# Kernel optimization log

Hardware: AMD Instinct MI355X
Metric: run time of the kernel (lower is better)

Reference implementation:

```python
import jax, jax.numpy as jnp
import numpy as np
from jax import lax

B, IMG, P, CIN = 8, 224, 16, 3
D, NH, E, HID, DEPTH, NC = 768, 12, 4, 3072, 12, 1000
NPAT = (IMG // P) ** 2  # 196
S = NPAT + 1            # 197 tokens incl cls
HD = D // NH            # 64
EPS = 1e-5


def _ln(x, g, b):
    m = jnp.mean(x, axis=-1, keepdims=True)
    v = jnp.mean((x - m) ** 2, axis=-1, keepdims=True)
    return (x - m) * lax.rsqrt(v + EPS) * g + b


def setup_inputs() -> dict:
    key = jax.random.key(0)
    ks = list(jax.random.split(key, 24))
    def rn(k, shape, s=0.02):
        return (jax.random.normal(k, shape) * s).astype(jnp.float32)
    inp = {
        "x": jax.random.normal(ks[0], (B, CIN, IMG, IMG), dtype=jnp.float32),
        "patch_w": rn(ks[1], (D, CIN, P, P)),
        "patch_b": jnp.zeros((D,), jnp.float32),
        "cls_token": jnp.zeros((1, 1, D), jnp.float32),
        "pos_embed": rn(ks[2], (1, S, D)),
        "ln1_g": jnp.ones((DEPTH, D), jnp.float32),
        "ln1_b": jnp.zeros((DEPTH, D), jnp.float32),
        "ln2_g": jnp.ones((DEPTH, D), jnp.float32),
        "ln2_b": jnp.zeros((DEPTH, D), jnp.float32),
        "attn_in_w": rn(ks[3], (DEPTH, 3 * D, D)),
        "attn_in_b": jnp.zeros((DEPTH, 3 * D), jnp.float32),
        "attn_out_w": rn(ks[4], (DEPTH, D, D)),
        "attn_out_b": jnp.zeros((DEPTH, D), jnp.float32),
        "gate_w": rn(ks[5], (DEPTH, E, D)),
        "gate_b": jnp.zeros((DEPTH, E), jnp.float32),
        "w1": rn(ks[6], (DEPTH, E, D, HID)),
        "b1": jnp.zeros((DEPTH, E, HID), jnp.float32),
        "w2": rn(ks[7], (DEPTH, E, HID, D)),
        "b2": jnp.zeros((DEPTH, E, D), jnp.float32),
        "head_w": rn(ks[8], (NC, D)),
        "head_b": jnp.zeros((NC,), jnp.float32),
    }
    return inp


def _forward(x, patch_w, patch_b, cls_token, pos_embed, ln1_g, ln1_b, ln2_g, ln2_b,
             attn_in_w, attn_in_b, attn_out_w, attn_out_b, gate_w, gate_b,
             w1, b1, w2, b2, head_w, head_b):
    # Patch embedding: conv stride=patch, then flatten spatial -> tokens
    feat = lax.conv_general_dilated(x, patch_w, window_strides=(P, P), padding="VALID",
                                    dimension_numbers=("NCHW", "OIHW", "NCHW"))
    t = feat.reshape(B, D, NPAT).transpose(0, 2, 1) + patch_b  # [B, 196, D]
    cls = jnp.broadcast_to(cls_token, (B, 1, D))
    h = jnp.concatenate([cls, t], axis=1) + pos_embed  # [B, S, D]

    scale = 1.0 / np.sqrt(HD).astype(np.float32)
    for i in range(DEPTH):
        # ---- attention (query = LN(x); key/value = x, as in source) ----
        qn = _ln(h, ln1_g[i], ln1_b[i])
        wq, wk, wv = attn_in_w[i, :D], attn_in_w[i, D:2 * D], attn_in_w[i, 2 * D:]
        bq, bk, bv = attn_in_b[i, :D], attn_in_b[i, D:2 * D], attn_in_b[i, 2 * D:]
        q = (qn @ wq.T + bq).reshape(B, S, NH, HD)
        k = (h @ wk.T + bk).reshape(B, S, NH, HD)
        v = (h @ wv.T + bv).reshape(B, S, NH, HD)
        scores = jnp.einsum("bqhd,bkhd->bhqk", q, k) * scale
        attn = jax.nn.softmax(scores, axis=-1)
        o = jnp.einsum("bhqk,bkhd->bqhd", attn, v).reshape(B, S, D)
        h = h + o @ attn_out_w[i].T + attn_out_b[i]

        # ---- Top-1 gated MoE MLP ----
        y = _ln(h, ln2_g[i], ln2_b[i])
        logits = y @ gate_w[i].T + gate_b[i]            # [B,S,E]
        probs = jax.nn.softmax(logits, axis=-1)
        top = jnp.argmax(probs, axis=-1)                # [B,S]
        onehot = jax.nn.one_hot(top, E, dtype=y.dtype)  # [B,S,E]
        gv = jnp.sum(probs * onehot, axis=-1)           # [B,S] top-1 gate score
        hidd = jax.nn.gelu(jnp.einsum("bsd,edh->besh", y, w1[i]) + b1[i][None, :, None, :])
        eout = jnp.einsum("besh,ehd->besd", hidd, w2[i]) + b2[i][None, :, None, :]
        moe = jnp.einsum("bse,besd->bsd", onehot, eout) * gv[..., None]
        h = h + moe

    return h[:, 0] @ head_w.T + head_b  # [B, NC]


def reference(x, patch_w, patch_b, cls_token, pos_embed, ln1_g, ln1_b, ln2_g, ln2_b,
              attn_in_w, attn_in_b, attn_out_w, attn_out_b, gate_w, gate_b,
              w1, b1, w2, b2, head_w, head_b):
    return _forward(x, patch_w, patch_b, cls_token, pos_embed, ln1_g, ln1_b, ln2_g,
                    ln2_b, attn_in_w, attn_in_b, attn_out_w, attn_out_b, gate_w,
                    gate_b, w1, b1, w2, b2, head_w, head_b)
```

## Files before the change

kernel.cpp:

```cpp
#include <hip/hip_runtime.h>
#include <math.h>


#define BB 8
#define SS 197
#define DD 768
#define MT (BB*SS)
#define NPATCH 196
#define MPE (BB*NPATCH)
#define HHID 3072
#define NEXP 4

typedef __bf16 bf16_t;
typedef bf16_t bf16x8 __attribute__((ext_vector_type(8)));
typedef float  f32x4  __attribute__((ext_vector_type(4)));

__device__ __forceinline__ void gload16(const bf16_t* g, bf16_t* l) {
    __builtin_amdgcn_global_load_lds(
        (const __attribute__((address_space(1))) unsigned int*)g,
        (__attribute__((address_space(3))) unsigned int*)l,
        16, 0, 0);
}

__device__ __forceinline__ bf16x8 cvt8(float4 a, float4 b) {
    bf16x8 o;
    o[0]=(bf16_t)a.x; o[1]=(bf16_t)a.y; o[2]=(bf16_t)a.z; o[3]=(bf16_t)a.w;
    o[4]=(bf16_t)b.x; o[5]=(bf16_t)b.y; o[6]=(bf16_t)b.z; o[7]=(bf16_t)b.w;
    return o;
}

__global__ void gather_patches(const float* __restrict__ x, bf16_t* __restrict__ Xp) {
    int i = blockIdx.x * 256 + threadIdx.x;
    if (i >= MPE * DD) return;
    int k = i % DD;
    int m = i / DD;
    int pw = k & 15, ph = (k >> 4) & 15, cin = k >> 8;
    int px = m % 14, py = (m / 14) % 14, b = m / NPATCH;
    int row = py * 16 + ph, col = px * 16 + pw;
    Xp[i] = (bf16_t)x[((size_t)(b * 3 + cin) * 224 + row) * 224 + col];
}

__global__ void build_h(const float* __restrict__ pe, const float* __restrict__ patch_b,
                        const float* __restrict__ cls, const float* __restrict__ pos,
                        float* __restrict__ h) {
    int i = blockIdx.x * 256 + threadIdx.x;
    if (i >= MT * DD) return;
    int d = i % DD;
    int s = (i / DD) % SS;
    int b = i / (DD * SS);
    float v;
    if (s == 0) v = cls[d];
    else        v = pe[((size_t)(b * NPATCH) + (s - 1)) * DD + d] + patch_b[d];
    h[i] = v + pos[s * DD + d];
}

__global__ void cvt_bf16(const float* __restrict__ in, bf16_t* __restrict__ out, int n) {
    int i = (blockIdx.x * 256 + threadIdx.x) * 8;
    if (i >= n) return;
    const float4* p = (const float4*)(in + i);
    *(bf16x8*)(out + i) = cvt8(p[0], p[1]);
}

__global__ __launch_bounds__(256) void transpose_cvt(const float* __restrict__ in,
                                                     bf16_t* __restrict__ out, int R, int C) {
    int z = blockIdx.z;
    in  += (size_t)z * R * C;
    out += (size_t)z * R * C;
    __shared__ float t[32][33];
    int c0 = blockIdx.x * 32, r0 = blockIdx.y * 32;
    int tx = threadIdx.x & 31, ty = threadIdx.x >> 5;
    #pragma unroll
    for (int i = 0; i < 4; i++)
        t[ty + 8*i][tx] = in[(size_t)(r0 + ty + 8*i) * C + c0 + tx];
    __syncthreads();
    #pragma unroll
    for (int i = 0; i < 4; i++)
        out[(size_t)(c0 + ty + 8*i) * R + r0 + tx] = (bf16_t)t[tx][ty + 8*i];
}

template<int MODE>
__global__ __launch_bounds__(256) void gemm_bf16(
    const bf16_t* __restrict__ A, const bf16_t* __restrict__ Bw,
    const float* __restrict__ bias, float* __restrict__ C, bf16_t* __restrict__ Cb,
    const int* __restrict__ cnt, const int* __restrict__ idx,
    const float* __restrict__ gv, int M, int N, int K)
{
    constexpr bool GATHER = (MODE == 3 || MODE == 4);
    int z = blockIdx.z;
    int count = GATHER ? cnt[z] : M;
    int m0 = blockIdx.y * 64;
    if (m0 >= count) return;
    int n0 = blockIdx.x * 64;
    Bw += (size_t)z * N * K;
    const float* biasz = bias ? (bias + (size_t)z * N) : nullptr;

    __shared__ bf16_t As[2][64 * 64];
    __shared__ bf16_t Bs[2][64 * 64];
    __shared__ int toks[64];

    int tid = threadIdx.x, lane = tid & 63, w = tid >> 6;
    if (tid < 64) {
        int mm = m0 + tid;
        if (mm > count - 1) mm = count - 1;
        toks[tid] = GATHER ? idx[z * MT + mm] : mm;
    }
    __syncthreads();

    int wm = (w >> 1) * 32, wn = (w & 1) * 32;
    int fr = lane & 15, fs = lane >> 4;

    f32x4 acc[2][2];
    #pragma unroll
    for (int mi = 0; mi < 2; mi++)
        #pragma unroll
        for (int ni = 0; ni < 2; ni++)
            #pragma unroll
            for (int j = 0; j < 4; j++) acc[mi][ni][j] = 0.f;

    int nk = K >> 6;

    #define STAGE(buf, k0)                                                          \
        {                                                                           \
            _Pragma("unroll")                                                       \
            for (int it = 0; it < 2; it++) {                                        \
                int row = 8*(it*4 + w) + (lane >> 3), cc = lane & 7;                \
                const bf16_t* sa = A  + (size_t)toks[row] * K + (k0) + ((cc ^ (row & 7)) << 3); \
                gload16(sa, &As[buf][(it*4 + w) * 512]);                            \
                const bf16_t* sb = Bw + (size_t)(n0 + row) * K + (k0) + ((cc ^ (row & 7)) << 3); \
                gload16(sb, &Bs[buf][(it*4 + w) * 512]);                            \
            }                                                                       \
        }

    STAGE(0, 0);
    __syncthreads();
    int cur = 0;
    for (int t = 0; t < nk; t++) {
        if (t + 1 < nk) STAGE(cur ^ 1, (t + 1) << 6);
        #pragma unroll
        for (int ks = 0; ks < 2; ks++) {
            bf16x8 af[2], bfr[2];
            #pragma unroll
            for (int mi = 0; mi < 2; mi++) {
                int r = wm + mi * 16 + fr;
                af[mi] = *(bf16x8*)&As[cur][r * 64 + (((fs + ks*4) ^ (r & 7)) << 3)];
            }
            #pragma unroll
            for (int ni = 0; ni < 2; ni++) {
                int r = wn + ni * 16 + fr;
                bfr[ni] = *(bf16x8*)&Bs[cur][r * 64 + (((fs + ks*4) ^ (r & 7)) << 3)];
            }
            #pragma unroll
            for (int mi = 0; mi < 2; mi++)
                #pragma unroll
                for (int ni = 0; ni < 2; ni++)
                    acc[mi][ni] = __builtin_amdgcn_mfma_f32_16x16x32_bf16(af[mi], bfr[ni], acc[mi][ni], 0, 0, 0);
        }
        __syncthreads();
        cur ^= 1;
    }
    #undef STAGE

    #pragma unroll
    for (int mi = 0; mi < 2; mi++) {
        #pragma unroll
        for (int j = 0; j < 4; j++) {
            int rr = wm + mi * 16 + fs * 4 + j;
            if (m0 + rr >= count) continue;
            int crow = toks[rr];
            #pragma unroll
            for (int ni = 0; ni < 2; ni++) {
                int col = n0 + wn + ni * 16 + fr;
                float v = acc[mi][ni][j];
                if (MODE >= 2) v += biasz[col];
                if (MODE == 0) C[(size_t)crow * N + col] = v;
                else if (MODE == 2) C[(size_t)crow * N + col] += v;
                else if (MODE == 3) {
                    float g = 0.5f * v * (1.0f + tanhf(0.7978845608028654f * (v + 0.044715f * v * v * v)));
                    Cb[(size_t)crow * N + col] = (bf16_t)g;
                } else if (MODE == 4) {
                    C[(size_t)crow * N + col] += v * gv[crow];
                } else {
                    Cb[(size_t)crow * N + col] = (bf16_t)v;
                }
            }
        }
    }
}

__global__ __launch_bounds__(256) void ln1_kernel(const float* __restrict__ x,
                                                  const float* __restrict__ g,
                                                  const float* __restrict__ b,
                                                  bf16_t* __restrict__ qn,
                                                  bf16_t* __restrict__ hb)
{
    int m = blockIdx.x, t = threadIdx.x;
    __shared__ float buf[DD];
    __shared__ float tmp[4];
    float s = 0.f;
    for (int j = t; j < DD; j += 256) { float v = x[(size_t)m*DD + j]; buf[j] = v; s += v; }
    #pragma unroll
    for (int o = 32; o > 0; o >>= 1) s += __shfl_down(s, o);
    if ((t & 63) == 0) tmp[t >> 6] = s;
    __syncthreads();
    float mean = (tmp[0]+tmp[1]+tmp[2]+tmp[3]) * (1.0f/DD);
    float s2 = 0.f;
    for (int j = t; j < DD; j += 256) { float d = buf[j] - mean; s2 += d*d; }
    #pragma unroll
    for (int o = 32; o > 0; o >>= 1) s2 += __shfl_down(s2, o);
    __syncthreads();
    if ((t & 63) == 0) tmp[t >> 6] = s2;
    __syncthreads();
    float var = (tmp[0]+tmp[1]+tmp[2]+tmp[3]) * (1.0f/DD);
    float rs = rsqrtf(var + 1e-5f);
    for (int j = t; j < DD; j += 256) {
        qn[(size_t)m*DD + j] = (bf16_t)((buf[j] - mean) * rs * g[j] + b[j]);
        hb[(size_t)m*DD + j] = (bf16_t)buf[j];
    }
}

__global__ __launch_bounds__(256) void ln2_gate_kernel(const float* __restrict__ x,
                                                       const float* __restrict__ g,
                                                       const float* __restrict__ b,
                                                       const float* __restrict__ gw,
                                                       const float* __restrict__ gb,
                                                       bf16_t* __restrict__ yb,
                                                       float* __restrict__ gv,
                                                       int* __restrict__ cnt,
                                                       int* __restrict__ idxb)
{
    int m = blockIdx.x, t = threadIdx.x;
    __shared__ float buf[DD];
    __shared__ float tmp[4];
    __shared__ float red[4][4];
    float s = 0.f;
    for (int j = t; j < DD; j += 256) { float v = x[(size_t)m*DD + j]; buf[j] = v; s += v; }
    #pragma unroll
    for (int o = 32; o > 0; o >>= 1) s += __shfl_down(s, o);
    if ((t & 63) == 0) tmp[t >> 6] = s;
    __syncthreads();
    float mean = (tmp[0]+tmp[1]+tmp[2]+tmp[3]) * (1.0f/DD);
    float s2 = 0.f;
    for (int j = t; j < DD; j += 256) { float d = buf[j] - mean; s2 += d*d; }
    #pragma unroll
    for (int o = 32; o > 0; o >>= 1) s2 += __shfl_down(s2, o);
    __syncthreads();
    if ((t & 63) == 0) tmp[t >> 6] = s2;
    __syncthreads();
    float var = (tmp[0]+tmp[1]+tmp[2]+tmp[3]) * (1.0f/DD);
    float rs = rsqrtf(var + 1e-5f);
    float p0 = 0.f, p1 = 0.f, p2 = 0.f, p3 = 0.f;
    for (int j = t; j < DD; j += 256) {
        float y = (buf[j] - mean) * rs * g[j] + b[j];
        yb[(size_t)m*DD + j] = (bf16_t)y;
        p0 += y * gw[j];
        p1 += y * gw[DD + j];
        p2 += y * gw[2*DD + j];
        p3 += y * gw[3*DD + j];
    }
    #pragma unroll
    for (int o = 32; o > 0; o >>= 1) {
        p0 += __shfl_down(p0, o); p1 += __shfl_down(p1, o);
        p2 += __shfl_down(p2, o); p3 += __shfl_down(p3, o);
    }
    if ((t & 63) == 0) { int ww = t >> 6; red[ww][0]=p0; red[ww][1]=p1; red[ww][2]=p2; red[ww][3]=p3; }
    __syncthreads();
    if (t == 0) {
        float l0 = red[0][0]+red[1][0]+red[2][0]+red[3][0] + gb[0];
        float l1 = red[0][1]+red[1][1]+red[2][1]+red[3][1] + gb[1];
        float l2 = red[0][2]+red[1][2]+red[2][2]+red[3][2] + gb[2];
        float l3 = red[0][3]+red[1][3]+red[2][3]+red[3][3] + gb[3];
        int top = 0; float best = l0;
        if (l1 > best) { best = l1; top = 1; }
        if (l2 > best) { best = l2; top = 2; }
        if (l3 > best) { best = l3; top = 3; }
        float Z = __expf(l0-best) + __expf(l1-best) + __expf(l2-best) + __expf(l3-best);
        gv[m] = 1.0f / Z;
        int pos = atomicAdd(&cnt[top], 1);
        idxb[top * MT + pos] = m;
    }
}

__global__ __launch_bounds__(256) void attn_kernel(const bf16_t* __restrict__ qb,
                                                   const bf16_t* __restrict__ kvb,
                                                   bf16_t* __restrict__ ob)
{
    int qt = blockIdx.x, hh = blockIdx.y, b = blockIdx.z;
    __shared__ bf16_t Qs[64 * 64];
    __shared__ bf16_t Ks[64 * 64];
    __shared__ bf16_t Vt[64 * 72];
    __shared__ float  Sc[64 * 276];
    __shared__ float  linv[64];

    int tid = threadIdx.x, lane = tid & 63, w = tid >> 6;
    int wm = (w >> 1) * 32, wn = (w & 1) * 32;
    int fr = lane & 15, fs = lane >> 4;

    #pragma unroll
    for (int it = 0; it < 2; it++) {
        int row = 8*(it*4 + w) + (lane >> 3), cc = lane & 7;
        int q = qt*64 + row; if (q > SS-1) q = SS-1;
        const bf16_t* src = qb + ((size_t)(b*SS + q))*DD + hh*64 + ((cc ^ (row & 7)) << 3);
        gload16(src, &Qs[(it*4 + w) * 512]);
    }

    for (int kt = 0; kt < 4; kt++) {
        __syncthreads();
        #pragma unroll
        for (int it = 0; it < 2; it++) {
            int row = 8*(it*4 + w) + (lane >> 3), cc = lane & 7;
            int k = kt*64 + row; if (k > SS-1) k = SS-1;
            const bf16_t* src = kvb + ((size_t)(b*SS + k))*1536 + hh*64 + ((cc ^ (row & 7)) << 3);
            gload16(src, &Ks[(it*4 + w) * 512]);
        }
        __syncthreads();
        f32x4 acc[2][2];
        #pragma unroll
        for (int mi = 0; mi < 2; mi++)
            #pragma unroll
            for (int ni = 0; ni < 2; ni++)
                #pragma unroll
                for (int j = 0; j < 4; j++) acc[mi][ni][j] = 0.f;
        #pragma unroll
        for (int ks = 0; ks < 2; ks++) {
            bf16x8 af[2], bfr[2];
            #pragma unroll
            for (int mi = 0; mi < 2; mi++) {
                int r = wm + mi * 16 + fr;
                af[mi] = *(bf16x8*)&Qs[r * 64 + (((fs + ks*4) ^ (r & 7)) << 3)];
            }
            #pragma unroll
            for (int ni = 0; ni < 2; ni++) {
                int r = wn + ni * 16 + fr;
                bfr[ni] = *(bf16x8*)&Ks[r * 64 + (((fs + ks*4) ^ (r & 7)) << 3)];
            }
            #pragma unroll
            for (int mi = 0; mi < 2; mi++)
                #pragma unroll
                for (int ni = 0; ni < 2; ni++)
                    acc[mi][ni] = __builtin_amdgcn_mfma_f32_16x16x32_bf16(af[mi], bfr[ni], acc[mi][ni], 0, 0, 0);
        }
        #pragma unroll
        for (int mi = 0; mi < 2; mi++)
            #pragma unroll
            for (int j = 0; j < 4; j++) {
                int qr = wm + mi * 16 + fs * 4 + j;
                #pragma unroll
                for (int ni = 0; ni < 2; ni++) {
                    int col = kt*64 + wn + ni * 16 + fr;
                    float v = acc[mi][ni][j] * 0.125f;
                    if (col > SS-1) v = -1e30f;
                    Sc[qr * 276 + col] = v;
                }
            }
    }
    __syncthreads();

    {
        int row = tid >> 2, c = tid & 3;
        float m = -1e30f;
        for (int i = c; i < 256; i += 4) m = fmaxf(m, Sc[row * 276 + i]);
        m = fmaxf(m, __shfl_xor(m, 1, 4));
        m = fmaxf(m, __shfl_xor(m, 2, 4));
        float s = 0.f;
        for (int i = c; i < 256; i += 4) {
            float e = __expf(Sc[row * 276 + i] - m);
            Sc[row * 276 + i] = e;
            s += e;
        }
        s += __shfl_xor(s, 1, 4);
        s += __shfl_xor(s, 2, 4);
        if (c == 0) linv[row] = 1.0f / s;
    }

    f32x4 pv[2][2];
    #pragma unroll
    for (int mi = 0; mi < 2; mi++)
        #pragma unroll
        for (int ni = 0; ni < 2; ni++)
            #pragma unroll
            for (int j = 0; j < 4; j++) pv[mi][ni][j] = 0.f;

    for (int kt = 0; kt < 4; kt++) {
        __syncthreads();
        {
            int s = tid >> 2, c2 = tid & 3;
            int k = kt*64 + s; if (k > SS-1) k = SS-1;
            const bf16_t* vr = kvb + ((size_t)(b*SS + k))*1536 + 768 + hh*64;
            bf16x8 v0 = *(const bf16x8*)(vr + c2*16);
            bf16x8 v1 = *(const bf16x8*)(vr + c2*16 + 8);
            #pragma unroll
            for (int j = 0; j < 8; j++) {
                Vt[(c2*16 + j) * 72 + s]     = v0[j];
                Vt[(c2*16 + 8 + j) * 72 + s] = v1[j];
            }
        }
        __syncthreads();
        #pragma unroll
        for (int ks = 0; ks < 2; ks++) {
            int s0 = kt*64 + ks*32;
            bf16x8 af[2], bfr[2];
            #pragma unroll
            for (int mi = 0; mi < 2; mi++) {
                int qr = wm + mi * 16 + fr;
                const float* p = &Sc[qr * 276 + s0 + fs * 8];
                af[mi] = cvt8(*(const float4*)p, *(const float4*)(p + 4));
            }
            #pragma unroll
            for (int ni = 0; ni < 2; ni++) {
                int d = wn + ni * 16 + fr;
                bfr[ni] = *(bf16x8*)&Vt[d * 72 + ks*32 + fs*8];
            }
            #pragma unroll
            for (int mi = 0; mi < 2; mi++)
                #pragma unroll
                for (int ni = 0; ni < 2; ni++)
                    pv[mi][ni] = __builtin_amdgcn_mfma_f32_16x16x32_bf16(af[mi], bfr[ni], pv[mi][ni], 0, 0, 0);
        }
    }

    #pragma unroll
    for (int mi = 0; mi < 2; mi++)
        #pragma unroll
        for (int j = 0; j < 4; j++) {
            int qr = wm + mi * 16 + fs * 4 + j;
            int q = qt*64 + qr;
            if (q > SS-1) continue;
            float il = linv[qr];
            #pragma unroll
            for (int ni = 0; ni < 2; ni++) {
                int d = wn + ni * 16 + fr;
                ob[((size_t)(b*SS + q))*DD + hh*64 + d] = (bf16_t)(pv[mi][ni][j] * il);
            }
        }
}

__global__ void zero_cnt(int* cnt) { if (threadIdx.x < NEXP) cnt[threadIdx.x] = 0; }

__global__ void head_kernel(const float* __restrict__ h, const float* __restrict__ hw,
                            const float* __restrict__ hb, float* __restrict__ out)
{
    int i = blockIdx.x * 256 + threadIdx.x;
    if (i >= BB * 1000) return;
    int b = i & 7, n = i >> 3;
    const float4* hr = (const float4*)(h + (size_t)(b * SS) * DD);
    const float4* wr = (const float4*)(hw + (size_t)n * DD);
    float s = 0.f;
    #pragma unroll 4
    for (int k = 0; k < DD/4; k++) {
        float4 a = hr[k], wv = wr[k];
        s += a.x*wv.x + a.y*wv.y + a.z*wv.z + a.w*wv.w;
    }
    out[b * 1000 + n] = s + hb[n];
}

extern "C" void kernel_launch(void* const* d_in, const int* in_sizes, int n_in,
                              void* d_out, int out_size, void* d_ws, size_t ws_size,
                              hipStream_t stream) {
    const float* x          = (const float*)d_in[0];
    const float* patch_w    = (const float*)d_in[1];
    const float* patch_b    = (const float*)d_in[2];
    const float* cls_token  = (const float*)d_in[3];
    const float* pos_embed  = (const float*)d_in[4];
    const float* ln1_g      = (const float*)d_in[5];
    const float* ln1_b      = (const float*)d_in[6];
    const float* ln2_g      = (const float*)d_in[7];
    const float* ln2_b      = (const float*)d_in[8];
    const float* attn_in_w  = (const float*)d_in[9];
    const float* attn_in_b  = (const float*)d_in[10];
    const float* attn_out_w = (const float*)d_in[11];
    const float* attn_out_b = (const float*)d_in[12];
    const float* gate_w     = (const float*)d_in[13];
    const float* gate_b     = (const float*)d_in[14];
    const float* w1         = (const float*)d_in[15];
    const float* b1         = (const float*)d_in[16];
    const float* w2         = (const float*)d_in[17];
    const float* b2         = (const float*)d_in[18];
    const float* head_w     = (const float*)d_in[19];
    const float* head_b     = (const float*)d_in[20];
    float* out = (float*)d_out;

    char* wsb = (char*)d_ws;
    auto alloc = [&](size_t bytes) { char* p = wsb; wsb += (bytes + 63) & ~63ULL; return p; };
    bf16_t* Xp    = (bf16_t*)alloc((size_t)MPE * DD * 2);
    float*  pe    = (float*) alloc((size_t)MPE * DD * 4);
    float*  h     = (float*) alloc((size_t)MT * DD * 4);
    bf16_t* qn_bf = (bf16_t*)alloc((size_t)MT * DD * 2);
    bf16_t* h_bf  = (bf16_t*)alloc((size_t)MT * DD * 2);
    bf16_t* qb_bf = (bf16_t*)alloc((size_t)MT * DD * 2);
    bf16_t* kv_bf = (bf16_t*)alloc((size_t)MT * 1536 * 2);
    bf16_t* ob_bf = (bf16_t*)alloc((size_t)MT * DD * 2);
    bf16_t* yb_bf = (bf16_t*)alloc((size_t)MT * DD * 2);
    bf16_t* hd_bf = (bf16_t*)alloc((size_t)MT * HHID * 2);
    float*  gv    = (float*) alloc((size_t)MT * 4);
    int*    cnt   = (int*)   alloc(64 * 4);
    int*    idxb  = (int*)   alloc((size_t)NEXP * MT * 4);
    bf16_t* wq_bf = (bf16_t*)alloc((size_t)2304 * DD * 2);
    bf16_t* wo_bf = (bf16_t*)alloc((size_t)DD * DD * 2);
    bf16_t* w1t   = (bf16_t*)alloc((size_t)NEXP * DD * HHID * 2);
    bf16_t* w2t   = (bf16_t*)alloc((size_t)NEXP * DD * HHID * 2);
    bf16_t* pw_bf = (bf16_t*)alloc((size_t)DD * DD * 2);

    dim3 blk(256);

    cvt_bf16<<<(DD*DD/8 + 255)/256, blk, 0, stream>>>(patch_w, pw_bf, DD*DD);
    gather_patches<<<(MPE*DD + 255)/256, blk, 0, stream>>>(x, Xp);
    gemm_bf16<0><<<dim3(DD/64, (MPE+63)/64, 1), blk, 0, stream>>>(
        Xp, pw_bf, nullptr, pe, nullptr, nullptr, nullptr, nullptr, MPE, DD, DD);
    build_h<<<(MT*DD + 255)/256, blk, 0, stream>>>(pe, patch_b, cls_token, pos_embed, h);

    for (int i = 0; i < 12; i++) {
        const float* aw    = attn_in_w  + (size_t)i * 2304 * DD;
        const float* ab    = attn_in_b  + (size_t)i * 2304;
        const float* ow    = attn_out_w + (size_t)i * DD * DD;
        const float* obias = attn_out_b + (size_t)i * DD;
        const float* l1g = ln1_g + (size_t)i * DD;
        const float* l1b = ln1_b + (size_t)i * DD;
        const float* l2g = ln2_g + (size_t)i * DD;
        const float* l2b = ln2_b + (size_t)i * DD;
        const float* gw  = gate_w + (size_t)i * NEXP * DD;
        const float* gb  = gate_b + (size_t)i * NEXP;
        const float* w1l = w1 + (size_t)i * NEXP * DD * HHID;
        const float* b1l = b1 + (size_t)i * NEXP * HHID;
        const float* w2l = w2 + (size_t)i * NEXP * HHID * DD;
        const float* b2l = b2 + (size_t)i * NEXP * DD;

        cvt_bf16<<<(2304*DD/8 + 255)/256, blk, 0, stream>>>(aw, wq_bf, 2304*DD);
        cvt_bf16<<<(DD*DD/8 + 255)/256, blk, 0, stream>>>(ow, wo_bf, DD*DD);
        transpose_cvt<<<dim3(HHID/32, DD/32, NEXP), blk, 0, stream>>>(w1l, w1t, DD, HHID);
        transpose_cvt<<<dim3(DD/32, HHID/32, NEXP), blk, 0, stream>>>(w2l, w2t, HHID, DD);

        ln1_kernel<<<MT, blk, 0, stream>>>(h, l1g, l1b, qn_bf, h_bf);
        gemm_bf16<5><<<dim3(DD/64, 25, 1), blk, 0, stream>>>(
            qn_bf, wq_bf, ab, nullptr, qb_bf, nullptr, nullptr, nullptr, MT, DD, DD);
        gemm_bf16<5><<<dim3(1536/64, 25, 1), blk, 0, stream>>>(
            h_bf, wq_bf + (size_t)DD * DD, ab + DD, nullptr, kv_bf, nullptr, nullptr, nullptr, MT, 1536, DD);
        attn_kernel<<<dim3(4, 12, BB), blk, 0, stream>>>(qb_bf, kv_bf, ob_bf);
        gemm_bf16<2><<<dim3(DD/64, 25, 1), blk, 0, stream>>>(
            ob_bf, wo_bf, obias, h, nullptr, nullptr, nullptr, nullptr, MT, DD, DD);
        zero_cnt<<<1, 64, 0, stream>>>(cnt);
        ln2_gate_kernel<<<MT, blk, 0, stream>>>(h, l2g, l2b, gw, gb, yb_bf, gv, cnt, idxb);
        gemm_bf16<3><<<dim3(HHID/64, 25, NEXP), blk, 0, stream>>>(
            yb_bf, w1t, b1l, nullptr, hd_bf, cnt, idxb, nullptr, MT, HHID, DD);
        gemm_bf16<4><<<dim3(DD/64, 25, NEXP), blk, 0, stream>>>(
            hd_bf, w2t, b2l, h, nullptr, cnt, idxb, gv, MT, DD, HHID);
    }

    head_kernel<<<(BB*1000 + 255)/256, blk, 0, stream>>>(h, head_w, head_b, out);
}
```

Before: 2.475 ms.

## Enlarge GEMM tiles to 128x64 and hoist all weight conversions before the layer loop

The GEMM kernel is templated on tile size and now uses 128x64 block tiles, with each wave computing 64x32 through four M fragments. This raises reuse of each loaded B fragment and halves the number of M blocks. All per-layer weight conversion and transpose launches move into single batched launches before the layer loop, using larger per-layer bf16 weight buffers and per-layer expert counters that are zeroed once. The trade-off is more workspace memory, more registers per thread, and worse tail occupancy for the small gathered expert GEMMs.

After: 2.718 ms. 1.1x slower.

```diff
diff --git a/kernel.cpp b/kernel.cpp
--- a/kernel.cpp
+++ b/kernel.cpp
@@ -78,57 +78,69 @@
         out[(size_t)(c0 + ty + 8*i) * R + r0 + tx] = (bf16_t)t[tx][ty + 8*i];
 }
 
-template<int MODE>
-__global__ __launch_bounds__(256) void gemm_bf16(
+template<int BM, int BN, int MODE>
+__global__ __launch_bounds__((BM/64)*(BN/32)*64) void gemm_bf16(
     const bf16_t* __restrict__ A, const bf16_t* __restrict__ Bw,
     const float* __restrict__ bias, float* __restrict__ C, bf16_t* __restrict__ Cb,
     const int* __restrict__ cnt, const int* __restrict__ idx,
     const float* __restrict__ gv, int M, int N, int K)
 {
+    constexpr int NW  = (BM/64)*(BN/32);
+    constexpr int WNC = BN/32;
+    constexpr int IA  = (BM/8)/NW;
+    constexpr int IB  = (BN/8)/NW;
     constexpr bool GATHER = (MODE == 3 || MODE == 4);
+
     int z = blockIdx.z;
     int count = GATHER ? cnt[z] : M;
-    int m0 = blockIdx.y * 64;
+    int m0 = blockIdx.y * BM;
     if (m0 >= count) return;
-    int n0 = blockIdx.x * 64;
+    int n0 = blockIdx.x * BN;
     Bw += (size_t)z * N * K;
     const float* biasz = bias ? (bias + (size_t)z * N) : nullptr;
 
-    __shared__ bf16_t As[2][64 * 64];
-    __shared__ bf16_t Bs[2][64 * 64];
-    __shared__ int toks[64];
+    __shared__ bf16_t As[2][BM * 64];
+    __shared__ bf16_t Bs[2][BN * 64];
+    __shared__ int toks[BM];
 
     int tid = threadIdx.x, lane = tid & 63, w = tid >> 6;
-    if (tid < 64) {
+    if (tid < BM) {
         int mm = m0 + tid;
         if (mm > count - 1) mm = count - 1;
         toks[tid] = GATHER ? idx[z * MT + mm] : mm;
     }
     __syncthreads();
 
-    int wm = (w >> 1) * 32, wn = (w & 1) * 32;
+    int wm = (w / WNC) * 64, wn = (w % WNC) * 32;
     int fr = lane & 15, fs = lane >> 4;
 
-    f32x4 acc[2][2];
-    #pragma unroll
-    for (int mi = 0; mi < 2; mi++)
+    f32x4 acc[4][2];
+    #pragma unroll
+    for (int mi = 0; mi < 4; mi++)
         #pragma unroll
         for (int ni = 0; ni < 2; ni++)
             #pragma unroll
             for (int j = 0; j < 4; j++) acc[mi][ni][j] = 0.f;
 
     int nk = K >> 6;
-
-    #define STAGE(buf, k0)                                                          \
-        {                                                                           \
-            _Pragma("unroll")                                                       \
-            for (int it = 0; it < 2; it++) {                                        \
-                int row = 8*(it*4 + w) + (lane >> 3), cc = lane & 7;                \
-                const bf16_t* sa = A  + (size_t)toks[row] * K + (k0) + ((cc ^ (row & 7)) << 3); \
-                gload16(sa, &As[buf][(it*4 + w) * 512]);                            \
-                const bf16_t* sb = Bw + (size_t)(n0 + row) * K + (k0) + ((cc ^ (row & 7)) << 3); \
-                gload16(sb, &Bs[buf][(it*4 + w) * 512]);                            \
-            }                                                                       \
+    int srow = lane >> 3, scc = lane & 7;
+
+    #define STAGE(buf, k0)                                                              \
+        {                                                                               \
+            _Pragma("unroll")                                                           \
+            for (int i = 0; i < IA; i++) {                                              \
+                int blk = i*NW + w;                                                     \
+                int row = blk*8 + srow;                                                 \
+                const bf16_t* s = A + (size_t)toks[row] * K + (k0) + ((scc ^ (row & 7)) << 3); \
+                gload16(s, &As[buf][blk * 512]);                                        \
+            }                                                                           \
+            _Pragma("unroll")                                                           \
+            for (int i = 0; i < IB; i++) {                                              \
+                int blk = i*NW + w;                                                     \
+                int row = blk*8 + srow;                                                 \
+                const bf16_t* s = Bw + (size_t)(n0 + row) * K + (k0) + ((scc ^ (row & 7)) << 3); \
+                gload16(s, &Bs[buf][blk * 512]);                                        \
+            }                                                                           \
         }
 
     STAGE(0, 0);
@@ -138,9 +150,9 @@
         if (t + 1 < nk) STAGE(cur ^ 1, (t + 1) << 6);
         #pragma unroll
         for (int ks = 0; ks < 2; ks++) {
-            bf16x8 af[2], bfr[2];
-            #pragma unroll
-            for (int mi = 0; mi < 2; mi++) {
+            bf16x8 af[4], bfr[2];
+            #pragma unroll
+            for (int mi = 0; mi < 4; mi++) {
                 int r = wm + mi * 16 + fr;
                 af[mi] = *(bf16x8*)&As[cur][r * 64 + (((fs + ks*4) ^ (r & 7)) << 3)];
             }
@@ -150,7 +162,7 @@
                 bfr[ni] = *(bf16x8*)&Bs[cur][r * 64 + (((fs + ks*4) ^ (r & 7)) << 3)];
             }
             #pragma unroll
-            for (int mi = 0; mi < 2; mi++)
+            for (int mi = 0; mi < 4; mi++)
                 #pragma unroll
                 for (int ni = 0; ni < 2; ni++)
                     acc[mi][ni] = __builtin_amdgcn_mfma_f32_16x16x32_bf16(af[mi], bfr[ni], acc[mi][ni], 0, 0, 0);
@@ -161,7 +173,7 @@
     #undef STAGE
 
     #pragma unroll
-    for (int mi = 0; mi < 2; mi++) {
+    for (int mi = 0; mi < 4; mi++) {
         #pragma unroll
         for (int j = 0; j < 4; j++) {
             int rr = wm + mi * 16 + fs * 4 + j;
@@ -434,7 +446,7 @@
         }
 }
 
-__global__ void zero_cnt(int* cnt) { if (threadIdx.x < NEXP) cnt[threadIdx.x] = 0; }
+__global__ void zero_cnt48(int* cnt) { if (threadIdx.x < 12*NEXP) cnt[threadIdx.x] = 0; }
 
 __global__ void head_kernel(const float* __restrict__ h, const float* __restrict__ hw,
                             const float* __restrict__ hb, float* __restrict__ out)
@@ -492,26 +504,34 @@
     bf16_t* yb_bf = (bf16_t*)alloc((size_t)MT * DD * 2);
     bf16_t* hd_bf = (bf16_t*)alloc((size_t)MT * HHID * 2);
     float*  gv    = (float*) alloc((size_t)MT * 4);
-    int*    cnt   = (int*)   alloc(64 * 4);
-    int*    idxb  = (int*)   alloc((size_t)NEXP * MT * 4);
-    bf16_t* wq_bf = (bf16_t*)alloc((size_t)2304 * DD * 2);
-    bf16_t* wo_bf = (bf16_t*)alloc((size_t)DD * DD * 2);
-    bf16_t* w1t   = (bf16_t*)alloc((size_t)NEXP * DD * HHID * 2);
-    bf16_t* w2t   = (bf16_t*)alloc((size_t)NEXP * DD * HHID * 2);
+    int*    cnt   = (int*)   alloc(12 * NEXP * 4);
+    int*    idxb  = (int*)   alloc((size_t)12 * NEXP * MT * 4);
     bf16_t* pw_bf = (bf16_t*)alloc((size_t)DD * DD * 2);
+    bf16_t* wq_a  = (bf16_t*)alloc((size_t)12 * 2304 * DD * 2);
+    bf16_t* wo_a  = (bf16_t*)alloc((size_t)12 * DD * DD * 2);
+    bf16_t* w1t_a = (bf16_t*)alloc((size_t)12 * NEXP * DD * HHID * 2);
+    bf16_t* w2t_a = (bf16_t*)alloc((size_t)12 * NEXP * DD * HHID * 2);
 
     dim3 blk(256);
 
+    zero_cnt48<<<1, 64, 0, stream>>>(cnt);
     cvt_bf16<<<(DD*DD/8 + 255)/256, blk, 0, stream>>>(patch_w, pw_bf, DD*DD);
+    cvt_bf16<<<(12*2304*DD/8 + 255)/256, blk, 0, stream>>>(attn_in_w, wq_a, 12*2304*DD);
+    cvt_bf16<<<(12*DD*DD/8 + 255)/256, blk, 0, stream>>>(attn_out_w, wo_a, 12*DD*DD);
+    transpose_cvt<<<dim3(HHID/32, DD/32, 12*NEXP), blk, 0, stream>>>(w1, w1t_a, DD, HHID);
+    transpose_cvt<<<dim3(DD/32, HHID/32, 12*NEXP), blk, 0, stream>>>(w2, w2t_a, HHID, DD);
+
     gather_patches<<<(MPE*DD + 255)/256, blk, 0, stream>>>(x, Xp);
-    gemm_bf16<0><<<dim3(DD/64, (MPE+63)/64, 1), blk, 0, stream>>>(
+    gemm_bf16<128,64,0><<<dim3(12, 13, 1), blk, 0, stream>>>(
         Xp, pw_bf, nullptr, pe, nullptr, nullptr, nullptr, nullptr, MPE, DD, DD);
     build_h<<<(MT*DD + 255)/256, blk, 0, stream>>>(pe, patch_b, cls_token, pos_embed, h);
 
     for (int i = 0; i < 12; i++) {
-        const float* aw    = attn_in_w  + (size_t)i * 2304 * DD;
+        const bf16_t* wq_bf = wq_a  + (size_t)i * 2304 * DD;
+        const bf16_t* wo_bf = wo_a  + (size_t)i * DD * DD;
+        const bf16_t* w1t   = w1t_a + (size_t)i * NEXP * DD * HHID;
+        const bf16_t* w2t   = w2t_a + (size_t)i * NEXP * DD * HHID;
         const float* ab    = attn_in_b  + (size_t)i * 2304;
-        const float* ow    = attn_out_w + (size_t)i * DD * DD;
         const float* obias = attn_out_b + (size_t)i * DD;
         const float* l1g = ln1_g + (size_t)i * DD;
         const float* l1b = ln1_b + (size_t)i * DD;
@@ -519,30 +539,24 @@
         const float* l2b = ln2_b + (size_t)i * DD;
         const float* gw  = gate_w + (size_t)i * NEXP * DD;
         const float* gb  = gate_b + (size_t)i * NEXP;
-        const float* w1l = w1 + (size_t)i * NEXP * DD * HHID;
         const float* b1l = b1 + (size_t)i * NEXP * HHID;
-        const float* w2l = w2 + (size_t)i * NEXP * HHID * DD;
         const float* b2l = b2 + (size_t)i * NEXP * DD;
-
-        cvt_bf16<<<(2304*DD/8 + 255)/256, blk, 0, stream>>>(aw, wq_bf, 2304*DD);
-        cvt_bf16<<<(DD*DD/8 + 255)/256, blk, 0, stream>>>(ow, wo_bf, DD*DD);
-        transpose_cvt<<<dim3(HHID/32, DD/32, NEXP), blk, 0, stream>>>(w1l, w1t, DD, HHID);
-        transpose_cvt<<<dim3(DD/32, HHID/32, NEXP), blk, 0, stream>>>(w2l, w2t, HHID, DD);
+        int* cnt_i  = cnt  + i * NEXP;
+        int* idxb_i = idxb + (size_t)i * NEXP * MT;
 
         ln1_kernel<<<MT, blk, 0, stream>>>(h, l1g, l1b, qn_bf, h_bf);
-        gemm_bf16<5><<<dim3(DD/64, 25, 1), blk, 0, stream>>>(
+        gemm_bf16<128,64,5><<<dim3(12, 13, 1), blk, 0, stream>>>(
             qn_bf, wq_bf, ab, nullptr, qb_bf, nullptr, nullptr, nullptr, MT, DD, DD);
-        gemm_bf16<5><<<dim3(1536/64, 25, 1), blk, 0, stream>>>(
+        gemm_bf16<128,64,5><<<dim3(24, 13, 1), blk, 0, stream>>>(
             h_bf, wq_bf + (size_t)DD * DD, ab + DD, nullptr, kv_bf, nullptr, nullptr, nullptr, MT, 1536, DD);
         attn_kernel<<<dim3(4, 12, BB), blk, 0, stream>>>(qb_bf, kv_bf, ob_bf);
-        gemm_bf16<2><<<dim3(DD/64, 25, 1), blk, 0, stream>>>(
+        gemm_bf16<128,64,2><<<dim3(12, 13, 1), blk, 0, stream>>>(
             ob_bf, wo_bf, obias, h, nullptr, nullptr, nullptr, nullptr, MT, DD, DD);
-        zero_cnt<<<1, 64, 0, stream>>>(cnt);
-        ln2_gate_kernel<<<MT, blk, 0, stream>>>(h, l2g, l2b, gw, gb, yb_bf, gv, cnt, idxb);
-        gemm_bf16<3><<<dim3(HHID/64, 25, NEXP), blk, 0, stream>>>(
-            yb_bf, w1t, b1l, nullptr, hd_bf, cnt, idxb, nullptr, MT, HHID, DD);
-        gemm_bf16<4><<<dim3(DD/64, 25, NEXP), blk, 0, stream>>>(
-            hd_bf, w2t, b2l, h, nullptr, cnt, idxb, gv, MT, DD, HHID);
+        ln2_gate_kernel<<<MT, blk, 0, stream>>>(h, l2g, l2b, gw, gb, yb_bf, gv, cnt_i, idxb_i);
+        gemm_bf16<128,64,3><<<dim3(48, 13, NEXP), blk, 0, stream>>>(
+            yb_bf, w1t, b1l, nullptr, hd_bf, cnt_i, idxb_i, nullptr, MT, HHID, DD);
+        gemm_bf16<128,64,4><<<dim3(12, 13, NEXP), blk, 0, stream>>>(
+            hd_bf, w2t, b2l, h, nullptr, cnt_i, idxb_i, gv, MT, DD, HHID);
     }
 
     head_kernel<<<(BB*1000 + 255)/256, blk, 0, stream>>>(h, head_w, head_b, out);
```
